# Kernel optimization log

Hardware: AMD Instinct MI355X
Metric: run time of the kernel (lower is better)

## Reference

```python
import jax, jax.numpy as jnp
import numpy as np

DIM = 256; SEQ = 2048; WIN = 64; HEADS = 4; RANK = 32; LAYERS = 3; VOCAB = 32000
EPS = 1e-6

def _unit(v):
    # unit_normalize_values: project onto unit sphere along feature dim
    return v / jnp.maximum(jnp.linalg.norm(v, axis=-1, keepdims=True), EPS)

def _signed_softmax(s):
    # signed_softmax_state: sign(s) * softmax(|s|) over nodes
    return jnp.sign(s) * jax.nn.softmax(jnp.abs(s), axis=-1)

def setup_inputs() -> dict:
    key = jax.random.key(0)
    ks = jax.random.split(key, 10)
    d = DIM
    return {
        "input_ids": jax.random.randint(ks[0], (2, SEQ), 0, VOCAB, dtype=jnp.int32),
        "emb": 0.02 * jax.random.normal(ks[1], (VOCAB, d), jnp.float32),
        "pos_emb": 0.02 * jax.random.normal(ks[2], (SEQ, d), jnp.float32),
        "anchor_val": 0.02 * jax.random.normal(ks[3], (d,), jnp.float32),
        "anchor_state": jnp.zeros((), jnp.float32),
        "Ws": 0.02 * jax.random.normal(ks[4], (d,), jnp.float32),
        "bs": jnp.zeros((), jnp.float32),
        "U": 0.02 * jax.random.normal(ks[5], (LAYERS, d, HEADS, RANK), jnp.float32),
        "V": 0.02 * jax.random.normal(ks[6], (LAYERS, d, HEADS, RANK), jnp.float32),
        "W1": 0.02 * jax.random.normal(ks[7], (LAYERS, d, 2 * d), jnp.float32),
        "b1": jnp.zeros((LAYERS, 2 * d), jnp.float32),
        "W2": 0.02 * jax.random.normal(ks[8], (LAYERS, 2 * d, d), jnp.float32),
        "b2": jnp.zeros((LAYERS, d), jnp.float32),
    }

def _forward(emb, pos_emb, anchor_val, anchor_state, Ws, bs, U, V, W1, b1, W2, b2, input_ids):
    B, S = input_ids.shape
    tok = emb[input_ids] + pos_emb[None, :S]          # [B,S,D]
    state_src = tok                                    # state projected from pre-unit-norm values
    tok = _unit(tok)
    tstate = state_src @ Ws + bs                       # [B,S] scalar state per node
    val = jnp.concatenate([jnp.broadcast_to(_unit(anchor_val), (B, 1, DIM)), tok], axis=1)
    state = jnp.concatenate([jnp.broadcast_to(anchor_state, (B, 1)), tstate], axis=1)
    N = S + 1
    offs = jnp.arange(-WIN, WIN + 1)
    idx = jnp.arange(N)[:, None] + offs[None, :]       # [N,K]
    valid = (idx >= 0) & (idx < N)
    idxc = jnp.clip(idx, 0, N - 1)
    inv_sqrt_r = np.float32(1.0 / np.sqrt(RANK))
    for l in range(LAYERS):
        q = jnp.einsum('bnd,dhr->bnhr', val, U[l])
        k = jnp.einsum('bnd,dhr->bnhr', val, V[l])
        knb = k[:, idxc]                               # [B,N,K,H,R] window gather
        s = jnp.einsum('bnhr,bnkhr->bnkh', q, knb) * inv_sqrt_r
        s = s.max(axis=-1)                             # max head-aggregate [B,N,K]
        a = jnp.where(valid, jnp.abs(s), -jnp.inf)
        wgt = jnp.where(valid, jnp.sign(s) * jax.nn.softmax(a, axis=-1), 0.0)  # signed-abs-softmax edges
        dval = jnp.einsum('bnk,bnkd->bnd', wgt, val[:, idxc])
        dstate = jnp.sum(wgt * state[:, idxc], axis=-1)
        # apply_delta: residual + norm(identity) + unit-norm + touched-mask where
        updated = val + dval
        nv = _unit(updated)
        touched = jnp.max(jnp.abs(jax.lax.stop_gradient(dval)), axis=-1, keepdims=True) > 0
        val = jnp.where(touched, nv, updated)
        state = _signed_softmax(state + dstate)
        # residual feed-forward then re-unit-norm
        h = jax.nn.gelu(jnp.einsum('bnd,dh->bnh', val, W1[l]) + b1[l], approximate=False)
        val = _unit(val + jnp.einsum('bnh,hd->bnd', h, W2[l]) + b2[l])
    return state, val

def reference(input_ids, emb, pos_emb, anchor_val, anchor_state, Ws, bs, U, V, W1, b1, W2, b2):
    return _forward(emb, pos_emb, anchor_val, anchor_state, Ws, bs, U, V, W1, b1, W2, b2, input_ids)
```

## Files before the change

kernel.cpp:

```cpp
#include <hip/hip_runtime.h>
#include <hip/hip_bf16.h>
#include <math.h>

#define BB 2
#define SS 2048
#define NN 2049
#define MM (BB*NN)
#define DD 256
#define HR 128
#define NHEAD 4
#define DFF 512
#define EPSF 1e-6f
#define TB8 257
#define EMB_BLKS 1025

typedef __attribute__((ext_vector_type(8))) short bf16x8;
typedef __attribute__((ext_vector_type(4))) float f32x4;

__device__ __forceinline__ float wave_sum(float v) {
    v += __shfl_down(v, 32, 64); v += __shfl_down(v, 16, 64);
    v += __shfl_down(v, 8, 64);  v += __shfl_down(v, 4, 64);
    v += __shfl_down(v, 2, 64);  v += __shfl_down(v, 1, 64);
    return v;
}
__device__ __forceinline__ float wave_max(float v) {
    v = fmaxf(v, __shfl_down(v, 32, 64)); v = fmaxf(v, __shfl_down(v, 16, 64));
    v = fmaxf(v, __shfl_down(v, 8, 64));  v = fmaxf(v, __shfl_down(v, 4, 64));
    v = fmaxf(v, __shfl_down(v, 2, 64));  v = fmaxf(v, __shfl_down(v, 1, 64));
    return v;
}
__device__ __forceinline__ float sgnf(float x) {
    return (x > 0.f) ? 1.f : ((x < 0.f) ? -1.f : 0.f);
}
__device__ __forceinline__ ushort f2b(float x) {
    __hip_bfloat16 h = __float2bfloat16(x);
    return *(ushort*)&h;
}
__device__ __forceinline__ float b2f(ushort u) {
    unsigned int v = ((unsigned int)u) << 16;
    return *(float*)&v;
}
__device__ __forceinline__ void split3(float x, ushort& h, ushort& m, ushort& l) {
    h = f2b(x);
    float r1 = x - b2f(h);
    m = f2b(r1);
    l = f2b(r1 - b2f(m));
}
__device__ __forceinline__ void pack_map(int e, int N, int& k, int& n) {
    int j = e & 7;
    int l = (e >> 3) & 63;
    int c = e >> 9;
    int ntiles = N >> 4;
    int kt = c / ntiles, nt = c - kt * ntiles;
    k = kt * 32 + ((l >> 4) << 3) + j;
    n = nt * 16 + (l & 15);
}


__device__ __forceinline__ void pack_job(int idx,
    const float* __restrict__ W1, const float* __restrict__ W2,
    const float* __restrict__ U,  const float* __restrict__ V,
    ushort* __restrict__ W1ph, ushort* __restrict__ W1pl,
    ushort* __restrict__ W2ph, ushort* __restrict__ W2pl,
    ushort* __restrict__ U0, ushort* __restrict__ U1, ushort* __restrict__ U2,
    ushort* __restrict__ V0, ushort* __restrict__ V1, ushort* __restrict__ V2)
{
    int l = idx / 327680;
    int r = idx - l * 327680;
    if (l >= 3) return;
    int k, n;
    if (r < 131072) {
        int e = r;
        pack_map(e, 512, k, n);
        float s = W1[(size_t)l * 131072 + (size_t)k * 512 + n];
        ushort h = f2b(s);
        W1ph[(size_t)l * 131072 + e] = h;
        W1pl[(size_t)l * 131072 + e] = f2b(s - b2f(h));
    } else if (r < 262144) {
        int e = r - 131072;
        pack_map(e, 256, k, n);
        float s = W2[(size_t)l * 131072 + (size_t)k * 256 + n];
        ushort h = f2b(s);
        W2ph[(size_t)l * 131072 + e] = h;
        W2pl[(size_t)l * 131072 + e] = f2b(s - b2f(h));
    } else if (r < 294912) {
        int e = r - 262144;
        pack_map(e, 128, k, n);
        ushort h, m, lo;
        split3(U[(size_t)l * 32768 + (size_t)k * 128 + n], h, m, lo);
        U0[(size_t)l * 32768 + e] = h;
        U1[(size_t)l * 32768 + e] = m;
        U2[(size_t)l * 32768 + e] = lo;
    } else {
        int e = r - 294912;
        pack_map(e, 128, k, n);
        ushort h, m, lo;
        split3(V[(size_t)l * 32768 + (size_t)k * 128 + n], h, m, lo);
        V0[(size_t)l * 32768 + e] = h;
        V1[(size_t)l * 32768 + e] = m;
        V2[(size_t)l * 32768 + e] = lo;
    }
}

__device__ __forceinline__ void state_job(int b, int t, float* red,
    const float* __restrict__ state_in, const float* __restrict__ dstate,
    float* __restrict__ state_out)
{
    float lmax = -INFINITY;
    for (int n = t; n < NN; n += 256) {
        float x = state_in[b * NN + n] + dstate[b * NN + n];
        lmax = fmaxf(lmax, fabsf(x));
    }
    lmax = wave_max(lmax);
    if ((t & 63) == 0) red[t >> 6] = lmax;
    __syncthreads();
    float m = fmaxf(fmaxf(red[0], red[1]), fmaxf(red[2], red[3]));
    float lsum = 0.f;
    for (int n = t; n < NN; n += 256)
        lsum += expf(fabsf(state_in[b * NN + n] + dstate[b * NN + n]) - m);
    lsum = wave_sum(lsum);
    __syncthreads();
    if ((t & 63) == 0) red[4 + (t >> 6)] = lsum;
    __syncthreads();
    float inv = 1.f / (red[4] + red[5] + red[6] + red[7]);
    for (int n = t; n < NN; n += 256) {
        float x = state_in[b * NN + n] + dstate[b * NN + n];
        state_out[b * NN + n] = sgnf(x) * expf(fabsf(x) - m) * inv;
    }
}


__global__ void pre_kernel(const int* __restrict__ ids, const float* __restrict__ emb,
                           const float* __restrict__ pos, const float* __restrict__ anchor_val,
                           const float* __restrict__ anchor_state, const float* __restrict__ Ws,
                           const float* __restrict__ bs, float* __restrict__ val,
                           float* __restrict__ state,
                           const float* __restrict__ W1, const float* __restrict__ W2,
                           const float* __restrict__ U,  const float* __restrict__ V,
                           ushort* W1ph, ushort* W1pl, ushort* W2ph, ushort* W2pl,
                           ushort* U0, ushort* U1, ushort* U2,
                           ushort* V0, ushort* V1, ushort* V2) {
    int bid = blockIdx.x;
    int t = threadIdx.x;
    if (bid < EMB_BLKS) {
        int w = t >> 6, l = t & 63;
        int row = bid * 4 + w;
        if (row >= MM) return;
        int b = row / NN, n = row % NN;
        f32x4 e;
        if (n == 0) {
            e = *(const f32x4*)(anchor_val + l * 4);
        } else {
            int id = ids[b * SS + (n - 1)];
            f32x4 em = *(const f32x4*)(emb + (size_t)id * DD + l * 4);
            f32x4 po = *(const f32x4*)(pos + (size_t)(n - 1) * DD + l * 4);
            e = em + po;
        }
        f32x4 wv = *(const f32x4*)(Ws + l * 4);
        float ss = e[0]*e[0] + e[1]*e[1] + e[2]*e[2] + e[3]*e[3];
        float ts = e[0]*wv[0] + e[1]*wv[1] + e[2]*wv[2] + e[3]*wv[3];
        #pragma unroll
        for (int off = 1; off < 64; off <<= 1) {
            ss += __shfl_xor(ss, off, 64);
            ts += __shfl_xor(ts, off, 64);
        }
        float rn = 1.f / fmaxf(sqrtf(ss), EPSF);
        f32x4 o;
        o[0] = e[0] * rn; o[1] = e[1] * rn; o[2] = e[2] * rn; o[3] = e[3] * rn;
        *(f32x4*)(val + (size_t)row * DD + l * 4) = o;
        if (l == 0) state[row] = (n == 0) ? anchor_state[0] : (ts + bs[0]);
        return;
    }
    int base = (bid - EMB_BLKS) * 1024 + t;
    #pragma unroll
    for (int k = 0; k < 4; k++)
        pack_job(base + k * 256, W1, W2, U, V,
                 W1ph, W1pl, W2ph, W2pl, U0, U1, U2, V0, V1, V2);
}


__global__ __launch_bounds__(256, 3)
void proj_kernel(const float* __restrict__ Xin,
                 const ushort* __restrict__ U0, const ushort* __restrict__ U1,
                 const ushort* __restrict__ U2,
                 const ushort* __restrict__ V0, const ushort* __restrict__ V1,
                 const ushort* __restrict__ V2,
                 ushort* __restrict__ q0, ushort* __restrict__ q1,
                 ushort* __restrict__ q2,
                 ushort* __restrict__ k0, ushort* __restrict__ k1,
                 ushort* __restrict__ k2) {
    __shared__ __align__(16) char smem[24576];
    int t = threadIdx.x;
    int w = t >> 6, l = t & 63;
    int lm = l & 15, quad = l >> 4;
    int m0 = blockIdx.x * 16;
    bool isQ = (blockIdx.y == 0);
    const ushort* P0 = isQ ? U0 : V0;
    const ushort* P1 = isQ ? U1 : V1;
    const ushort* P2 = isQ ? U2 : V2;

    #pragma unroll
    for (int rr = 0; rr < 4; rr++) {
        int row = w * 4 + rr;
        int tok = m0 + row; if (tok > MM - 1) tok = MM - 1;
        f32x4 x = *(const f32x4*)(Xin + (size_t)tok * DD + l * 4);
        ushort4 h4, m4, l4;
        ushort hh, mm, ll;
        split3(x[0], hh, mm, ll); h4.x = hh; m4.x = mm; l4.x = ll;
        split3(x[1], hh, mm, ll); h4.y = hh; m4.y = mm; l4.y = ll;
        split3(x[2], hh, mm, ll); h4.z = hh; m4.z = mm; l4.z = ll;
        split3(x[3], hh, mm, ll); h4.w = hh; m4.w = mm; l4.w = ll;
        unsigned byte = ((unsigned)(row * 512 + l * 8)) ^ ((unsigned)((row & 7) << 4));
        *(ushort4*)(smem + 0 * 8192 + byte) = h4;
        *(ushort4*)(smem + 1 * 8192 + byte) = m4;
        *(ushort4*)(smem + 2 * 8192 + byte) = l4;
    }
    __syncthreads();

    f32x4 acc[2];
    acc[0] = (f32x4)(0.f); acc[1] = (f32x4)(0.f);
    #pragma unroll
    for (int kt = 0; kt < 8; kt++) {
        unsigned abyte = ((unsigned)(lm * 512 + kt * 64 + quad * 16)) ^
                         ((unsigned)((lm & 7) << 4));
        bf16x8 a0 = *(const bf16x8*)(smem + 0 * 8192 + abyte);
        bf16x8 a1 = *(const bf16x8*)(smem + 1 * 8192 + abyte);
        bf16x8 a2 = *(const bf16x8*)(smem + 2 * 8192 + abyte);
        #pragma unroll
        for (int jj = 0; jj < 2; jj++) {
            int ntl = w * 2 + jj;
            size_t off = ((size_t)(kt * 8 + ntl) * 64 + l) * 8;
            bf16x8 b0 = *(const bf16x8*)(P0 + off);
            bf16x8 b1 = *(const bf16x8*)(P1 + off);
            bf16x8 b2 = *(const bf16x8*)(P2 + off);
            acc[jj] = __builtin_amdgcn_mfma_f32_16x16x32_bf16(a0, b0, acc[jj], 0, 0, 0);
            acc[jj] = __builtin_amdgcn_mfma_f32_16x16x32_bf16(a0, b1, acc[jj], 0, 0, 0);
            acc[jj] = __builtin_amdgcn_mfma_f32_16x16x32_bf16(a1, b0, acc[jj], 0, 0, 0);
            acc[jj] = __builtin_amdgcn_mfma_f32_16x16x32_bf16(a1, b1, acc[jj], 0, 0, 0);
            acc[jj] = __builtin_amdgcn_mfma_f32_16x16x32_bf16(a0, b2, acc[jj], 0, 0, 0);
            acc[jj] = __builtin_amdgcn_mfma_f32_16x16x32_bf16(a2, b0, acc[jj], 0, 0, 0);
        }
    }
    ushort* o0 = isQ ? q0 : k0;
    ushort* o1 = isQ ? q1 : k1;
    ushort* o2 = isQ ? q2 : k2;
    #pragma unroll
    for (int jj = 0; jj < 2; jj++) {
        int n = (w * 2 + jj) * 16 + lm;
        #pragma unroll
        for (int r = 0; r < 4; r++) {
            int tok = m0 + quad * 4 + r;
            if (tok < MM) {
                ushort h, m, lo;
                split3(acc[jj][r], h, m, lo);
                size_t oi = (size_t)tok * HR + n;
                o0[oi] = h; o1[oi] = m; o2[oi] = lo;
            }
        }
    }
}


__global__ __launch_bounds__(256, 3)
void attn_kernel(const float* __restrict__ val_in,
                 const float* __restrict__ state_in,
                 const ushort* __restrict__ q0, const ushort* __restrict__ q1,
                 const ushort* __restrict__ q2,
                 const ushort* __restrict__ k0, const ushort* __restrict__ k1,
                 const ushort* __restrict__ k2,
                 float* __restrict__ val_out,
                 ushort* __restrict__ vbH, ushort* __restrict__ vbM,
                 float* __restrict__ dstate_out) {
    __shared__ float sc4[NHEAD][8][148];
    __shared__ float wgt2[144][12];
    __shared__ float redS[8][4];
    __shared__ float redM[8][4];

    int b = blockIdx.x / TB8;
    int n0 = (blockIdx.x % TB8) * 8;
    int t = threadIdx.x;
    int w = t >> 6, l = t & 63;
    int lm = l & 15, quad = l >> 4;

    {
        int qrow = n0 + (lm & 7);
        if (qrow > NN - 1) qrow = NN - 1;
        size_t qa = ((size_t)(b * NN + qrow)) * HR + w * 32 + quad * 8;
        bf16x8 a0 = *(const bf16x8*)(q0 + qa);
        bf16x8 a1 = *(const bf16x8*)(q1 + qa);
        bf16x8 a2 = *(const bf16x8*)(q2 + qa);
        #pragma unroll
        for (int jt = 0; jt < 9; jt++) {
            int j = n0 - 64 + jt * 16 + lm;
            j = (j < 0) ? 0 : ((j > NN - 1) ? NN - 1 : j);
            size_t ka = ((size_t)(b * NN + j)) * HR + w * 32 + quad * 8;
            bf16x8 kf0 = *(const bf16x8*)(k0 + ka);
            bf16x8 kf1 = *(const bf16x8*)(k1 + ka);
            bf16x8 kf2 = *(const bf16x8*)(k2 + ka);
            f32x4 acc = (f32x4)(0.f);
            acc = __builtin_amdgcn_mfma_f32_16x16x32_bf16(a0, kf0, acc, 0, 0, 0);
            acc = __builtin_amdgcn_mfma_f32_16x16x32_bf16(a0, kf1, acc, 0, 0, 0);
            acc = __builtin_amdgcn_mfma_f32_16x16x32_bf16(a1, kf0, acc, 0, 0, 0);
            acc = __builtin_amdgcn_mfma_f32_16x16x32_bf16(a1, kf1, acc, 0, 0, 0);
            acc = __builtin_amdgcn_mfma_f32_16x16x32_bf16(a0, kf2, acc, 0, 0, 0);
            acc = __builtin_amdgcn_mfma_f32_16x16x32_bf16(a2, kf0, acc, 0, 0, 0);
            if (quad < 2) {
                #pragma unroll
                for (int r = 0; r < 4; r++)
                    sc4[w][quad * 4 + r][jt * 16 + lm] = acc[r];
            }
        }
    }
    __syncthreads();

    {
        int m = t >> 5, p = t & 31;
        int n = n0 + m;
        bool tokv = (n < NN);
        float sv[5]; bool vv[5];
        float mx = -INFINITY;
        #pragma unroll
        for (int i = 0; i < 5; i++) {
            int tap = p + 32 * i;
            bool inb = (tap < 144);
            int tapc = inb ? tap : 0;
            int j = n0 - 64 + tapc;
            float s0 = sc4[0][m][tapc], s1 = sc4[1][m][tapc];
            float s2 = sc4[2][m][tapc], s3 = sc4[3][m][tapc];
            float s = fmaxf(fmaxf(s0, s1), fmaxf(s2, s3)) * 0.17677669529663687f;
            bool v = inb && tokv && (tap >= m) && (tap <= m + 128) && (j >= 0) && (j < NN);
            sv[i] = s; vv[i] = v;
            if (v) mx = fmaxf(mx, fabsf(s));
        }
        for (int off = 16; off > 0; off >>= 1) mx = fmaxf(mx, __shfl_xor(mx, off, 64));
        float ee[5];
        float sum = 0.f;
        #pragma unroll
        for (int i = 0; i < 5; i++) {
            ee[i] = vv[i] ? expf(fabsf(sv[i]) - mx) : 0.f;
            sum += ee[i];
        }
        for (int off = 16; off > 0; off >>= 1) sum += __shfl_xor(sum, off, 64);
        float inv = (sum > 0.f) ? 1.f / sum : 0.f;
        float ds = 0.f;
        #pragma unroll
        for (int i = 0; i < 5; i++) {
            int tap = p + 32 * i;
            if (tap < 144) {
                float wg = vv[i] ? sgnf(sv[i]) * ee[i] * inv : 0.f;
                wgt2[tap][m] = wg;
                if (vv[i]) ds += wg * state_in[b * NN + (n0 - 64 + tap)];
            }
        }
        for (int off = 16; off > 0; off >>= 1) ds += __shfl_xor(ds, off, 64);
        if (p == 0 && tokv) dstate_out[b * NN + n] = ds;
    }
    __syncthreads();

    {
        int d = (t >> 2) * 4;
        int tg = t & 3;
        int tok0 = tg * 2, tok1 = tg * 2 + 1;
        int jlo = (n0 >= 64) ? 0 : (64 - n0);
        int jhi = NN - 1 - n0 + 64; if (jhi > 135) jhi = 135;
        const float* vbase = val_in + ((size_t)(b * NN + n0 - 64)) * DD + d;
        f32x4 acc0 = (f32x4)(0.f), acc1 = (f32x4)(0.f);
        int jj = jlo;
        for (; jj + 3 <= jhi; jj += 4) {
            f32x4 v0 = *(const f32x4*)(vbase + (size_t)(jj + 0) * DD);
            f32x4 v1 = *(const f32x4*)(vbase + (size_t)(jj + 1) * DD);
            f32x4 v2 = *(const f32x4*)(vbase + (size_t)(jj + 2) * DD);
            f32x4 v3 = *(const f32x4*)(vbase + (size_t)(jj + 3) * DD);
            float wa0 = wgt2[jj + 0][tok0], wa1 = wgt2[jj + 0][tok1];
            float wb0 = wgt2[jj + 1][tok0], wb1 = wgt2[jj + 1][tok1];
            float wc0 = wgt2[jj + 2][tok0], wc1 = wgt2[jj + 2][tok1];
            float wd0 = wgt2[jj + 3][tok0], wd1 = wgt2[jj + 3][tok1];
            #pragma unroll
            for (int c = 0; c < 4; c++) {
                acc0[c] += v0[c] * wa0 + v1[c] * wb0 + v2[c] * wc0 + v3[c] * wd0;
                acc1[c] += v0[c] * wa1 + v1[c] * wb1 + v2[c] * wc1 + v3[c] * wd1;
            }
        }
        for (; jj <= jhi; jj++) {
            f32x4 v = *(const f32x4*)(vbase + (size_t)jj * DD);
            float w0 = wgt2[jj][tok0], w1 = wgt2[jj][tok1];
            #pragma unroll
            for (int c = 0; c < 4; c++) {
                acc0[c] += v[c] * w0;
                acc1[c] += v[c] * w1;
            }
        }
        f32x4 u[2]; f32x4 ac[2]; ac[0] = acc0; ac[1] = acc1;
        #pragma unroll
        for (int ti = 0; ti < 2; ti++) {
            int tok = tg * 2 + ti;
            int n = n0 + tok;
            f32x4 vold = (f32x4)(0.f);
            if (n < NN) vold = *(const f32x4*)(val_in + ((size_t)(b * NN + n)) * DD + d);
            u[ti] = vold + ac[ti];
            float s = u[ti][0]*u[ti][0] + u[ti][1]*u[ti][1] + u[ti][2]*u[ti][2] + u[ti][3]*u[ti][3];
            float mb = fmaxf(fmaxf(fabsf(ac[ti][0]), fabsf(ac[ti][1])),
                             fmaxf(fabsf(ac[ti][2]), fabsf(ac[ti][3])));
            for (int off = 4; off <= 32; off <<= 1) {
                s += __shfl_xor(s, off, 64);
                mb = fmaxf(mb, __shfl_xor(mb, off, 64));
            }
            if ((l >> 2) == 0) { redS[tok][w] = s; redM[tok][w] = mb; }
        }
        __syncthreads();
        #pragma unroll
        for (int ti = 0; ti < 2; ti++) {
            int tok = tg * 2 + ti;
            int n = n0 + tok;
            if (n < NN) {
                float ss = redS[tok][0] + redS[tok][1] + redS[tok][2] + redS[tok][3];
                float mab = fmaxf(fmaxf(redM[tok][0], redM[tok][1]),
                                  fmaxf(redM[tok][2], redM[tok][3]));
                float rn = 1.f / fmaxf(sqrtf(ss), EPSF);
                f32x4 o = u[ti];
                if (mab > 0.f) { o[0] *= rn; o[1] *= rn; o[2] *= rn; o[3] *= rn; }
                size_t oi = ((size_t)(b * NN + n)) * DD + d;
                *(f32x4*)(val_out + oi) = o;
                ushort4 hv, mv;
                {
                    ushort h0 = f2b(o[0]); hv.x = h0; mv.x = f2b(o[0] - b2f(h0));
                    ushort h1 = f2b(o[1]); hv.y = h1; mv.y = f2b(o[1] - b2f(h1));
                    ushort h2 = f2b(o[2]); hv.z = h2; mv.z = f2b(o[2] - b2f(h2));
                    ushort h3 = f2b(o[3]); hv.w = h3; mv.w = f2b(o[3] - b2f(h3));
                }
                *(ushort4*)(vbH + oi) = hv;
                *(ushort4*)(vbM + oi) = mv;
            }
        }
    }
}


__global__ __launch_bounds__(1024, 1)
void fusedF_kernel(const ushort* __restrict__ vb0, const ushort* __restrict__ vb1,
                   const float*  __restrict__ valB,
                   const ushort* __restrict__ W1h, const ushort* __restrict__ W1l,
                   const float*  __restrict__ b1,
                   const ushort* __restrict__ W2h, const ushort* __restrict__ W2l,
                   const float*  __restrict__ b2,
                   const ushort* __restrict__ U0, const ushort* __restrict__ U1,
                   const ushort* __restrict__ U2,
                   const ushort* __restrict__ V0, const ushort* __restrict__ V1,
                   const ushort* __restrict__ V2,
                   ushort* __restrict__ q0, ushort* __restrict__ q1,
                   ushort* __restrict__ q2,
                   ushort* __restrict__ k0, ushort* __restrict__ k1,
                   ushort* __restrict__ k2,
                   float* __restrict__ valA,
                   const float* __restrict__ s_in, const float* __restrict__ dstate,
                   float* __restrict__ s_out,
                   float* __restrict__ out2, int last)
{
    __shared__ __align__(16) char smem[98304];
    int t = threadIdx.x;
    int bid = blockIdx.x;

    if (bid >= 129) {
        if (bid - 129 < BB) {
            if (t < 256) {
                state_job(bid - 129, t, (float*)smem, s_in, dstate, s_out);
            } else {
                __syncthreads(); __syncthreads(); __syncthreads();
            }
        }
        return;
    }

    int g  = t >> 9;
    int tl = t & 511;
    int w = tl >> 6, l = tl & 63;
    int lm = l & 15, quad = l >> 4;
    int m0 = bid * 32 + g * 16;
    int row0 = m0 + lm; if (row0 > MM - 1) row0 = MM - 1;
    char* Hh_s = smem + g * 16384;
    char* Hl_s = smem + 32768 + g * 16384;
    char* Y_s  = smem + 65536 + g * 16384;
    char* P_s  = smem + g * 24576;

    {
        const ushort* xh = vb0 + (size_t)row0 * DD + quad * 8;
        const ushort* xm = vb1 + (size_t)row0 * DD + quad * 8;
        f32x4 acc[4];
        #pragma unroll
        for (int jj = 0; jj < 4; jj++) acc[jj] = (f32x4)(0.f);
        #pragma unroll
        for (int kt = 0; kt < 8; kt++) {
            bf16x8 ah = *(const bf16x8*)(xh + kt * 32);
            bf16x8 am = *(const bf16x8*)(xm + kt * 32);
            #pragma unroll
            for (int jj = 0; jj < 4; jj++) {
                int nt = w * 4 + jj;
                size_t off = ((size_t)(kt * 32 + nt) * 64 + l) * 8;
                bf16x8 bh = *(const bf16x8*)(W1h + off);
                bf16x8 bl = *(const bf16x8*)(W1l + off);
                acc[jj] = __builtin_amdgcn_mfma_f32_16x16x32_bf16(ah, bh, acc[jj], 0, 0, 0);
                acc[jj] = __builtin_amdgcn_mfma_f32_16x16x32_bf16(am, bh, acc[jj], 0, 0, 0);
                acc[jj] = __builtin_amdgcn_mfma_f32_16x16x32_bf16(ah, bl, acc[jj], 0, 0, 0);
            }
        }
        #pragma unroll
        for (int jj = 0; jj < 4; jj++) {
            int gn = (w * 4 + jj) * 16 + lm;
            float bb = b1[gn];
            #pragma unroll
            for (int r = 0; r < 4; r++) {
                int rho = quad * 4 + r;
                float x = acc[jj][r] + bb;
                float gl = 0.5f * x * (1.f + erff(x * 0.70710678118654752f));
                ushort gh = f2b(gl);
                unsigned byte = ((unsigned)(rho * 1024 + gn * 2)) ^
                                ((unsigned)((rho & 7) << 4));
                *(ushort*)(Hh_s + byte) = gh;
                *(ushort*)(Hl_s + byte) = f2b(gl - b2f(gh));
            }
        }
    }
    __syncthreads();

    {
        f32x4 acc[2];
        acc[0] = (f32x4)(0.f); acc[1] = (f32x4)(0.f);
        #pragma unroll
        for (int kt = 0; kt < 16; kt++) {
            unsigned ab = ((unsigned)(lm * 1024 + kt * 64 + quad * 16)) ^
                          ((unsigned)((lm & 7) << 4));
            bf16x8 ah = *(const bf16x8*)(Hh_s + ab);
            bf16x8 al = *(const bf16x8*)(Hl_s + ab);
            #pragma unroll
            for (int jj = 0; jj < 2; jj++) {
                int nt = w * 2 + jj;
                size_t off = ((size_t)(kt * 16 + nt) * 64 + l) * 8;
                bf16x8 bh = *(const bf16x8*)(W2h + off);
                bf16x8 bl = *(const bf16x8*)(W2l + off);
                acc[jj] = __builtin_amdgcn_mfma_f32_16x16x32_bf16(ah, bh, acc[jj], 0, 0, 0);
                acc[jj] = __builtin_amdgcn_mfma_f32_16x16x32_bf16(al, bh, acc[jj], 0, 0, 0);
                acc[jj] = __builtin_amdgcn_mfma_f32_16x16x32_bf16(ah, bl, acc[jj], 0, 0, 0);
            }
        }
        #pragma unroll
        for (int jj = 0; jj < 2; jj++) {
            int gn = (w * 2 + jj) * 16 + lm;
            float bb = b2[gn];
            #pragma unroll
            for (int r = 0; r < 4; r++) {
                int rho = quad * 4 + r;
                int tok = m0 + rho;
                int tokc = (tok > MM - 1) ? (MM - 1) : tok;
                float y = valB[(size_t)tokc * DD + gn] + acc[jj][r] + bb;
                unsigned byte = ((unsigned)(rho * 1024 + gn * 4)) ^
                                ((unsigned)((rho & 7) << 4));
                *(float*)(Y_s + byte) = y;
            }
        }
    }
    __syncthreads();

    if (last) {
        #pragma unroll
        for (int rr = 0; rr < 2; rr++) {
            int row = w * 2 + rr;
            int tok = m0 + row;
            unsigned byte = ((unsigned)(row * 1024 + l * 16)) ^
                            ((unsigned)((row & 7) << 4));
            f32x4 y = *(const f32x4*)(Y_s + byte);
            float s = y[0]*y[0] + y[1]*y[1] + y[2]*y[2] + y[3]*y[3];
            #pragma unroll
            for (int off = 1; off < 64; off <<= 1) s += __shfl_xor(s, off, 64);
            float rn = 1.f / fmaxf(sqrtf(s), EPSF);
            if (tok < MM) {
                f32x4 o;
                o[0] = y[0] * rn; o[1] = y[1] * rn; o[2] = y[2] * rn; o[3] = y[3] * rn;
                *(f32x4*)(out2 + (size_t)tok * DD + l * 4) = o;
            }
        }
        return;
    }

    #pragma unroll
    for (int rr = 0; rr < 2; rr++) {
        int row = w * 2 + rr;
        int tok = m0 + row;
        unsigned ybyte = ((unsigned)(row * 1024 + l * 16)) ^
                         ((unsigned)((row & 7) << 4));
        f32x4 x = *(const f32x4*)(Y_s + ybyte);
        float s = x[0]*x[0] + x[1]*x[1] + x[2]*x[2] + x[3]*x[3];
        #pragma unroll
        for (int off = 1; off < 64; off <<= 1) s += __shfl_xor(s, off, 64);
        float rn = 1.f / fmaxf(sqrtf(s), EPSF);
        x[0] *= rn; x[1] *= rn; x[2] *= rn; x[3] *= rn;
        if (tok < MM) *(f32x4*)(valA + (size_t)tok * DD + l * 4) = x;
        ushort4 h4, m4, l4;
        ushort hh, mm, ll;
        split3(x[0], hh, mm, ll); h4.x = hh; m4.x = mm; l4.x = ll;
        split3(x[1], hh, mm, ll); h4.y = hh; m4.y = mm; l4.y = ll;
        split3(x[2], hh, mm, ll); h4.z = hh; m4.z = mm; l4.z = ll;
        split3(x[3], hh, mm, ll); h4.w = hh; m4.w = mm; l4.w = ll;
        unsigned pbyte = ((unsigned)(row * 512 + l * 8)) ^ ((unsigned)((row & 7) << 4));
        *(ushort4*)(P_s + 0 * 8192 + pbyte) = h4;
        *(ushort4*)(P_s + 1 * 8192 + pbyte) = m4;
        *(ushort4*)(P_s + 2 * 8192 + pbyte) = l4;
    }
    __syncthreads();

    {
        f32x4 aq = (f32x4)(0.f), ak = (f32x4)(0.f);
        #pragma unroll
        for (int kt = 0; kt < 8; kt++) {
            unsigned abyte = ((unsigned)(lm * 512 + kt * 64 + quad * 16)) ^
                             ((unsigned)((lm & 7) << 4));
            bf16x8 a0 = *(const bf16x8*)(P_s + 0 * 8192 + abyte);
            bf16x8 a1 = *(const bf16x8*)(P_s + 1 * 8192 + abyte);
            bf16x8 a2 = *(const bf16x8*)(P_s + 2 * 8192 + abyte);
            size_t off = ((size_t)(kt * 8 + w) * 64 + l) * 8;
            bf16x8 u0 = *(const bf16x8*)(U0 + off);
            bf16x8 u1 = *(const bf16x8*)(U1 + off);
            bf16x8 u2 = *(const bf16x8*)(U2 + off);
            bf16x8 v0 = *(const bf16x8*)(V0 + off);
            bf16x8 v1 = *(const bf16x8*)(V1 + off);
            bf16x8 v2 = *(const bf16x8*)(V2 + off);
            aq = __builtin_amdgcn_mfma_f32_16x16x32_bf16(a0, u0, aq, 0, 0, 0);
            ak = __builtin_amdgcn_mfma_f32_16x16x32_bf16(a0, v0, ak, 0, 0, 0);
            aq = __builtin_amdgcn_mfma_f32_16x16x32_bf16(a0, u1, aq, 0, 0, 0);
            ak = __builtin_amdgcn_mfma_f32_16x16x32_bf16(a0, v1, ak, 0, 0, 0);
            aq = __builtin_amdgcn_mfma_f32_16x16x32_bf16(a1, u0, aq, 0, 0, 0);
            ak = __builtin_amdgcn_mfma_f32_16x16x32_bf16(a1, v0, ak, 0, 0, 0);
            aq = __builtin_amdgcn_mfma_f32_16x16x32_bf16(a1, u1, aq, 0, 0, 0);
            ak = __builtin_amdgcn_mfma_f32_16x16x32_bf16(a1, v1, ak, 0, 0, 0);
            aq = __builtin_amdgcn_mfma_f32_16x16x32_bf16(a0, u2, aq, 0, 0, 0);
            ak = __builtin_amdgcn_mfma_f32_16x16x32_bf16(a0, v2, ak, 0, 0, 0);
            aq = __builtin_amdgcn_mfma_f32_16x16x32_bf16(a2, u0, aq, 0, 0, 0);
            ak = __builtin_amdgcn_mfma_f32_16x16x32_bf16(a2, v0, ak, 0, 0, 0);
        }
        int n = w * 16 + lm;
        #pragma unroll
        for (int r = 0; r < 4; r++) {
            int tok = m0 + quad * 4 + r;
            if (tok < MM) {
                ushort h, m, lo;
                size_t oi = (size_t)tok * HR + n;
                split3(aq[r], h, m, lo);
                q0[oi] = h; q1[oi] = m; q2[oi] = lo;
                split3(ak[r], h, m, lo);
                k0[oi] = h; k1[oi] = m; k2[oi] = lo;
            }
        }
    }
}


extern "C" void kernel_launch(void* const* d_in, const int* in_sizes, int n_in,
                              void* d_out, int out_size, void* d_ws, size_t ws_size,
                              hipStream_t stream) {
    const int*   ids          = (const int*)d_in[0];
    const float* emb          = (const float*)d_in[1];
    const float* pos          = (const float*)d_in[2];
    const float* anchor_val   = (const float*)d_in[3];
    const float* anchor_state = (const float*)d_in[4];
    const float* Ws           = (const float*)d_in[5];
    const float* bs           = (const float*)d_in[6];
    const float* U            = (const float*)d_in[7];
    const float* V            = (const float*)d_in[8];
    const float* W1           = (const float*)d_in[9];
    const float* b1           = (const float*)d_in[10];
    const float* W2           = (const float*)d_in[11];
    const float* b2           = (const float*)d_in[12];
    float* out = (float*)d_out;

    ushort* p = (ushort*)d_ws;
    ushort* vB0 = p; p += (size_t)MM * DD;
    ushort* vB1 = p; p += (size_t)MM * DD;
    ushort* q0b = p; p += (size_t)MM * HR;
    ushort* q1b = p; p += (size_t)MM * HR;
    ushort* q2b = p; p += (size_t)MM * HR;
    ushort* k0b = p; p += (size_t)MM * HR;
    ushort* k1b = p; p += (size_t)MM * HR;
    ushort* k2b = p; p += (size_t)MM * HR;
    ushort* W1ph = p; p += 3 * 131072;
    ushort* W1pl = p; p += 3 * 131072;
    ushort* W2ph = p; p += 3 * 131072;
    ushort* W2pl = p; p += 3 * 131072;
    ushort* U0p = p; p += 3 * 32768;
    ushort* U1p = p; p += 3 * 32768;
    ushort* U2p = p; p += 3 * 32768;
    ushort* V0p = p; p += 3 * 32768;
    ushort* V1p = p; p += 3 * 32768;
    ushort* V2p = p; p += 3 * 32768;
    float* f = (float*)p;
    float* valA = f; f += (size_t)MM * DD;
    float* valB = f; f += (size_t)MM * DD;
    float* st0  = f; f += MM;
    float* st1  = f; f += MM;
    float* dst  = f; f += MM;

    pre_kernel<<<EMB_BLKS + 960, 256, 0, stream>>>(ids, emb, pos, anchor_val, anchor_state,
                                                   Ws, bs, valA, st0,
                                                   W1, W2, U, V,
                                                   W1ph, W1pl, W2ph, W2pl,
                                                   U0p, U1p, U2p, V0p, V1p, V2p);
    proj_kernel<<<dim3(257, 2), 256, 0, stream>>>(
        valA, U0p, U1p, U2p, V0p, V1p, V2p,
        q0b, q1b, q2b, k0b, k1b, k2b);

    float* s_in = st0;
    float* s_out = st1;
    for (int l = 0; l < 3; l++) {
        attn_kernel<<<BB * TB8, 256, 0, stream>>>(valA, s_in,
                                                  q0b, q1b, q2b, k0b, k1b, k2b,
                                                  valB, vB0, vB1, dst);
        int ln = (l < 2) ? (l + 1) : 0;
        fusedF_kernel<<<131, 1024, 0, stream>>>(
            vB0, vB1, valB,
            W1ph + (size_t)l * 131072, W1pl + (size_t)l * 131072, b1 + (size_t)l * DFF,
            W2ph + (size_t)l * 131072, W2pl + (size_t)l * 131072, b2 + (size_t)l * DD,
            U0p + (size_t)ln * 32768, U1p + (size_t)ln * 32768, U2p + (size_t)ln * 32768,
            V0p + (size_t)ln * 32768, V1p + (size_t)ln * 32768, V2p + (size_t)ln * 32768,
            q0b, q1b, q2b, k0b, k1b, k2b,
            valA,
            s_in, dst, (l == 2) ? out : s_out,
            out + MM, (l == 2) ? 1 : 0);
        float* tmp = s_in; s_in = s_out; s_out = tmp;
    }
}
```

Before: 298.6 us.

## Fuse attention and feed-forward per layer into one kernel via shared memory

Merges the windowed attention kernel and the fused feed-forward/projection kernel into one 1024-thread layer kernel. Each block runs four attention tiles of 8 tokens and stages the updated values and their bf16 hi/mid splits in shared memory for the FFN and next-layer Q/K projection, so the valB/vB0/vB1 global round trip is gone. Q/K and value buffers are now double-buffered, because other blocks still read the previous layer's neighbours. The state softmax moves into a separate small kernel. In exchange, only 129 blocks of 1024 threads run, with about 129KB of shared memory each, which cuts the parallelism available to the attention phase.

```diff
diff --git a/kernel.cpp b/kernel.cpp
--- a/kernel.cpp
+++ b/kernel.cpp
@@ -12,6 +12,8 @@
 #define DFF 512
 #define EPSF 1e-6f
 #define TB8 257
+#define NTILE 514
+#define MBLK 129
 #define EMB_BLKS 1025
 
 typedef __attribute__((ext_vector_type(8))) short bf16x8;
@@ -261,31 +263,53 @@
 }
 
 
-__global__ __launch_bounds__(256, 3)
-void attn_kernel(const float* __restrict__ val_in,
-                 const float* __restrict__ state_in,
-                 const ushort* __restrict__ q0, const ushort* __restrict__ q1,
-                 const ushort* __restrict__ q2,
-                 const ushort* __restrict__ k0, const ushort* __restrict__ k1,
-                 const ushort* __restrict__ k2,
-                 float* __restrict__ val_out,
-                 ushort* __restrict__ vbH, ushort* __restrict__ vbM,
-                 float* __restrict__ dstate_out) {
-    __shared__ float sc4[NHEAD][8][148];
-    __shared__ float wgt2[144][12];
-    __shared__ float redS[8][4];
-    __shared__ float redM[8][4];
-
-    int b = blockIdx.x / TB8;
-    int n0 = (blockIdx.x % TB8) * 8;
+__global__ void state_kernel(const float* __restrict__ s_in,
+                             const float* __restrict__ dstate,
+                             float* __restrict__ s_out) {
+    __shared__ float red[8];
+    state_job(blockIdx.x, threadIdx.x, red, s_in, dstate, s_out);
+}
+
+
+__global__ __launch_bounds__(1024, 1)
+void layer_kernel(const float* __restrict__ valA, const float* __restrict__ s_in,
+                  const ushort* __restrict__ q0, const ushort* __restrict__ q1,
+                  const ushort* __restrict__ q2,
+                  const ushort* __restrict__ k0, const ushort* __restrict__ k1,
+                  const ushort* __restrict__ k2,
+                  const ushort* __restrict__ W1h, const ushort* __restrict__ W1l,
+                  const float*  __restrict__ b1,
+                  const ushort* __restrict__ W2h, const ushort* __restrict__ W2l,
+                  const float*  __restrict__ b2,
+                  const ushort* __restrict__ U0, const ushort* __restrict__ U1,
+                  const ushort* __restrict__ U2,
+                  const ushort* __restrict__ V0, const ushort* __restrict__ V1,
+                  const ushort* __restrict__ V2,
+                  ushort* __restrict__ oq0, ushort* __restrict__ oq1,
+                  ushort* __restrict__ oq2,
+                  ushort* __restrict__ ok0, ushort* __restrict__ ok1,
+                  ushort* __restrict__ ok2,
+                  float* __restrict__ valA_out, float* __restrict__ dstate_out,
+                  float* __restrict__ out2, int last)
+{
+    __shared__ __align__(16) char smem[132096];
     int t = threadIdx.x;
-    int w = t >> 6, l = t & 63;
-    int lm = l & 15, quad = l >> 4;
+    int bid = blockIdx.x;
+
+    int tb4 = t >> 8;
+    int tl  = t & 255;
+    int tile = 4 * bid + tb4;
+    int treal = (tile < NTILE) ? tile : (NTILE - 1);
+    int batt = (treal >= 257) ? 1 : 0;
+    int n0 = (treal - batt * 257) * 8;
 
     {
+        float* sc4 = (float*)(smem + tb4 * 18944);
+        int w = tl >> 6, l = tl & 63;
+        int lm = l & 15, quad = l >> 4;
         int qrow = n0 + (lm & 7);
         if (qrow > NN - 1) qrow = NN - 1;
-        size_t qa = ((size_t)(b * NN + qrow)) * HR + w * 32 + quad * 8;
+        size_t qa = ((size_t)(batt * NN + qrow)) * HR + w * 32 + quad * 8;
         bf16x8 a0 = *(const bf16x8*)(q0 + qa);
         bf16x8 a1 = *(const bf16x8*)(q1 + qa);
         bf16x8 a2 = *(const bf16x8*)(q2 + qa);
@@ -293,7 +317,7 @@
         for (int jt = 0; jt < 9; jt++) {
             int j = n0 - 64 + jt * 16 + lm;
             j = (j < 0) ? 0 : ((j > NN - 1) ? NN - 1 : j);
-            size_t ka = ((size_t)(b * NN + j)) * HR + w * 32 + quad * 8;
+            size_t ka = ((size_t)(batt * NN + j)) * HR + w * 32 + quad * 8;
             bf16x8 kf0 = *(const bf16x8*)(k0 + ka);
             bf16x8 kf1 = *(const bf16x8*)(k1 + ka);
             bf16x8 kf2 = *(const bf16x8*)(k2 + ka);
@@ -307,14 +331,16 @@
             if (quad < 2) {
                 #pragma unroll
                 for (int r = 0; r < 4; r++)
-                    sc4[w][quad * 4 + r][jt * 16 + lm] = acc[r];
+                    sc4[((size_t)w * 8 + quad * 4 + r) * 148 + jt * 16 + lm] = acc[r];
             }
         }
     }
     __syncthreads();
 
     {
-        int m = t >> 5, p = t & 31;
+        float* sc4  = (float*)(smem + tb4 * 18944);
+        float* wgt2 = (float*)(smem + 75776 + tb4 * 6912);
+        int m = tl >> 5, p = tl & 31;
         int n = n0 + m;
         bool tokv = (n < NN);
         float sv[5]; bool vv[5];
@@ -325,8 +351,8 @@
             bool inb = (tap < 144);
             int tapc = inb ? tap : 0;
             int j = n0 - 64 + tapc;
-            float s0 = sc4[0][m][tapc], s1 = sc4[1][m][tapc];
-            float s2 = sc4[2][m][tapc], s3 = sc4[3][m][tapc];
+            float s0 = sc4[(0 * 8 + m) * 148 + tapc], s1 = sc4[(1 * 8 + m) * 148 + tapc];
+            float s2 = sc4[(2 * 8 + m) * 148 + tapc], s3 = sc4[(3 * 8 + m) * 148 + tapc];
             float s = fmaxf(fmaxf(s0, s1), fmaxf(s2, s3)) * 0.17677669529663687f;
             bool v = inb && tokv && (tap >= m) && (tap <= m + 128) && (j >= 0) && (j < NN);
             sv[i] = s; vv[i] = v;
@@ -348,22 +374,26 @@
             int tap = p + 32 * i;
             if (tap < 144) {
                 float wg = vv[i] ? sgnf(sv[i]) * ee[i] * inv : 0.f;
-                wgt2[tap][m] = wg;
-                if (vv[i]) ds += wg * state_in[b * NN + (n0 - 64 + tap)];
+                wgt2[tap * 12 + m] = wg;
+                if (vv[i]) ds += wg * s_in[batt * NN + (n0 - 64 + tap)];
             }
         }
         for (int off = 16; off > 0; off >>= 1) ds += __shfl_xor(ds, off, 64);
-        if (p == 0 && tokv) dstate_out[b * NN + n] = ds;
+        if (p == 0 && tokv && tile < NTILE) dstate_out[batt * NN + n] = ds;
     }
     __syncthreads();
 
     {
-        int d = (t >> 2) * 4;
-        int tg = t & 3;
+        float* wgt2 = (float*)(smem + 75776 + tb4 * 6912);
+        float* redS = (float*)(smem + 131072 + tb4 * 256);
+        float* redM = redS + 32;
+        int w = tl >> 6, l = tl & 63;
+        int d = (tl >> 2) * 4;
+        int tg = tl & 3;
         int tok0 = tg * 2, tok1 = tg * 2 + 1;
         int jlo = (n0 >= 64) ? 0 : (64 - n0);
         int jhi = NN - 1 - n0 + 64; if (jhi > 135) jhi = 135;
-        const float* vbase = val_in + ((size_t)(b * NN + n0 - 64)) * DD + d;
+        const float* vbase = valA + ((size_t)(batt * NN + n0 - 64)) * DD + d;
         f32x4 acc0 = (f32x4)(0.f), acc1 = (f32x4)(0.f);
         int jj = jlo;
         for (; jj + 3 <= jhi; jj += 4) {
@@ -371,10 +401,10 @@
             f32x4 v1 = *(const f32x4*)(vbase + (size_t)(jj + 1) * DD);
             f32x4 v2 = *(const f32x4*)(vbase + (size_t)(jj + 2) * DD);
             f32x4 v3 = *(const f32x4*)(vbase + (size_t)(jj + 3) * DD);
-            float wa0 = wgt2[jj + 0][tok0], wa1 = wgt2[jj + 0][tok1];
-            float wb0 = wgt2[jj + 1][tok0], wb1 = wgt2[jj + 1][tok1];
-            float wc0 = wgt2[jj + 2][tok0], wc1 = wgt2[jj + 2][tok1];
-            float wd0 = wgt2[jj + 3][tok0], wd1 = wgt2[jj + 3][tok1];
+            float wa0 = wgt2[(jj + 0) * 12 + tok0], wa1 = wgt2[(jj + 0) * 12 + tok1];
+            float wb0 = wgt2[(jj + 1) * 12 + tok0], wb1 = wgt2[(jj + 1) * 12 + tok1];
+            float wc0 = wgt2[(jj + 2) * 12 + tok0], wc1 = wgt2[(jj + 2) * 12 + tok1];
+            float wd0 = wgt2[(jj + 3) * 12 + tok0], wd1 = wgt2[(jj + 3) * 12 + tok1];
             #pragma unroll
             for (int c = 0; c < 4; c++) {
                 acc0[c] += v0[c] * wa0 + v1[c] * wb0 + v2[c] * wc0 + v3[c] * wd0;
@@ -383,7 +413,7 @@
         }
         for (; jj <= jhi; jj++) {
             f32x4 v = *(const f32x4*)(vbase + (size_t)jj * DD);
-            float w0 = wgt2[jj][tok0], w1 = wgt2[jj][tok1];
+            float w0 = wgt2[jj * 12 + tok0], w1 = wgt2[jj * 12 + tok1];
             #pragma unroll
             for (int c = 0; c < 4; c++) {
                 acc0[c] += v[c] * w0;
@@ -396,7 +426,7 @@
             int tok = tg * 2 + ti;
             int n = n0 + tok;
             f32x4 vold = (f32x4)(0.f);
-            if (n < NN) vold = *(const f32x4*)(val_in + ((size_t)(b * NN + n)) * DD + d);
+            if (n < NN) vold = *(const f32x4*)(valA + ((size_t)(batt * NN + n)) * DD + d);
             u[ti] = vold + ac[ti];
             float s = u[ti][0]*u[ti][0] + u[ti][1]*u[ti][1] + u[ti][2]*u[ti][2] + u[ti][3]*u[ti][3];
             float mb = fmaxf(fmaxf(fabsf(ac[ti][0]), fabsf(ac[ti][1])),
@@ -405,93 +435,60 @@
                 s += __shfl_xor(s, off, 64);
                 mb = fmaxf(mb, __shfl_xor(mb, off, 64));
             }
-            if ((l >> 2) == 0) { redS[tok][w] = s; redM[tok][w] = mb; }
+            if ((l >> 2) == 0) { redS[tok * 4 + w] = s; redM[tok * 4 + w] = mb; }
         }
         __syncthreads();
         #pragma unroll
         for (int ti = 0; ti < 2; ti++) {
             int tok = tg * 2 + ti;
+            int slot = tb4 * 8 + tok;
             int n = n0 + tok;
+            f32x4 o = (f32x4)(0.f);
             if (n < NN) {
-                float ss = redS[tok][0] + redS[tok][1] + redS[tok][2] + redS[tok][3];
-                float mab = fmaxf(fmaxf(redM[tok][0], redM[tok][1]),
-                                  fmaxf(redM[tok][2], redM[tok][3]));
+                float ss = redS[tok * 4 + 0] + redS[tok * 4 + 1] + redS[tok * 4 + 2] + redS[tok * 4 + 3];
+                float mab = fmaxf(fmaxf(redM[tok * 4 + 0], redM[tok * 4 + 1]),
+                                  fmaxf(redM[tok * 4 + 2], redM[tok * 4 + 3]));
                 float rn = 1.f / fmaxf(sqrtf(ss), EPSF);
-                f32x4 o = u[ti];
+                o = u[ti];
                 if (mab > 0.f) { o[0] *= rn; o[1] *= rn; o[2] *= rn; o[3] *= rn; }
-                size_t oi = ((size_t)(b * NN + n)) * DD + d;
-                *(f32x4*)(val_out + oi) = o;
-                ushort4 hv, mv;
-                {
-                    ushort h0 = f2b(o[0]); hv.x = h0; mv.x = f2b(o[0] - b2f(h0));
-                    ushort h1 = f2b(o[1]); hv.y = h1; mv.y = f2b(o[1] - b2f(h1));
-                    ushort h2 = f2b(o[2]); hv.z = h2; mv.z = f2b(o[2] - b2f(h2));
-                    ushort h3 = f2b(o[3]); hv.w = h3; mv.w = f2b(o[3] - b2f(h3));
-                }
-                *(ushort4*)(vbH + oi) = hv;
-                *(ushort4*)(vbM + oi) = mv;
-            }
-        }
-    }
-}
-
-
-__global__ __launch_bounds__(1024, 1)
-void fusedF_kernel(const ushort* __restrict__ vb0, const ushort* __restrict__ vb1,
-                   const float*  __restrict__ valB,
-                   const ushort* __restrict__ W1h, const ushort* __restrict__ W1l,
-                   const float*  __restrict__ b1,
-                   const ushort* __restrict__ W2h, const ushort* __restrict__ W2l,
-                   const float*  __restrict__ b2,
-                   const ushort* __restrict__ U0, const ushort* __restrict__ U1,
-                   const ushort* __restrict__ U2,
-                   const ushort* __restrict__ V0, const ushort* __restrict__ V1,
-                   const ushort* __restrict__ V2,
-                   ushort* __restrict__ q0, ushort* __restrict__ q1,
-                   ushort* __restrict__ q2,
-                   ushort* __restrict__ k0, ushort* __restrict__ k1,
-                   ushort* __restrict__ k2,
-                   float* __restrict__ valA,
-                   const float* __restrict__ s_in, const float* __restrict__ dstate,
-                   float* __restrict__ s_out,
-                   float* __restrict__ out2, int last)
-{
-    __shared__ __align__(16) char smem[98304];
-    int t = threadIdx.x;
-    int bid = blockIdx.x;
-
-    if (bid >= 129) {
-        if (bid - 129 < BB) {
-            if (t < 256) {
-                state_job(bid - 129, t, (float*)smem, s_in, dstate, s_out);
-            } else {
-                __syncthreads(); __syncthreads(); __syncthreads();
-            }
-        }
-        return;
-    }
-
-    int g  = t >> 9;
-    int tl = t & 511;
-    int w = tl >> 6, l = tl & 63;
+            }
+            unsigned vbb = ((unsigned)(slot * 1024 + d * 4)) ^ ((unsigned)((slot & 7) << 4));
+            *(f32x4*)(smem + vbb) = o;
+            ushort4 hv, mv;
+            {
+                ushort h0 = f2b(o[0]); hv.x = h0; mv.x = f2b(o[0] - b2f(h0));
+                ushort h1 = f2b(o[1]); hv.y = h1; mv.y = f2b(o[1] - b2f(h1));
+                ushort h2 = f2b(o[2]); hv.z = h2; mv.z = f2b(o[2] - b2f(h2));
+                ushort h3 = f2b(o[3]); hv.w = h3; mv.w = f2b(o[3] - b2f(h3));
+            }
+            unsigned pb = ((unsigned)(slot * 512 + d * 2)) ^ ((unsigned)((slot & 7) << 4));
+            *(ushort4*)(smem + 32768 + pb) = hv;
+            *(ushort4*)(smem + 49152 + pb) = mv;
+        }
+    }
+    __syncthreads();
+
+    int g   = t >> 9;
+    int tg2 = t & 511;
+    int w = tg2 >> 6, l = tg2 & 63;
     int lm = l & 15, quad = l >> 4;
-    int m0 = bid * 32 + g * 16;
-    int row0 = m0 + lm; if (row0 > MM - 1) row0 = MM - 1;
-    char* Hh_s = smem + g * 16384;
-    char* Hl_s = smem + 32768 + g * 16384;
-    char* Y_s  = smem + 65536 + g * 16384;
-    char* P_s  = smem + g * 24576;
+    char* Hh_s = smem + 65536 + g * 16384;
+    char* Hl_s = smem + 98304 + g * 16384;
+    char* Y_s  = smem + 32768 + g * 16384;
+    char* P_s  = smem + 65536 + g * 24576;
 
     {
-        const ushort* xh = vb0 + (size_t)row0 * DD + quad * 8;
-        const ushort* xm = vb1 + (size_t)row0 * DD + quad * 8;
+        int slot = g * 16 + lm;
+        unsigned sxor = (unsigned)((slot & 7) << 4);
+        unsigned vb0b = (unsigned)(slot * 512);
         f32x4 acc[4];
         #pragma unroll
         for (int jj = 0; jj < 4; jj++) acc[jj] = (f32x4)(0.f);
         #pragma unroll
         for (int kt = 0; kt < 8; kt++) {
-            bf16x8 ah = *(const bf16x8*)(xh + kt * 32);
-            bf16x8 am = *(const bf16x8*)(xm + kt * 32);
+            unsigned ab = (vb0b + kt * 64 + quad * 16) ^ sxor;
+            bf16x8 ah = *(const bf16x8*)(smem + 32768 + ab);
+            bf16x8 am = *(const bf16x8*)(smem + 49152 + ab);
             #pragma unroll
             for (int jj = 0; jj < 4; jj++) {
                 int nt = w * 4 + jj;
@@ -549,9 +546,10 @@
             #pragma unroll
             for (int r = 0; r < 4; r++) {
                 int rho = quad * 4 + r;
-                int tok = m0 + rho;
-                int tokc = (tok > MM - 1) ? (MM - 1) : tok;
-                float y = valB[(size_t)tokc * DD + gn] + acc[jj][r] + bb;
+                int slot = g * 16 + rho;
+                unsigned rb = ((unsigned)(slot * 1024 + gn * 4)) ^
+                              ((unsigned)((slot & 7) << 4));
+                float y = *(const float*)(smem + rb) + acc[jj][r] + bb;
                 unsigned byte = ((unsigned)(rho * 1024 + gn * 4)) ^
                                 ((unsigned)((rho & 7) << 4));
                 *(float*)(Y_s + byte) = y;
@@ -564,7 +562,13 @@
         #pragma unroll
         for (int rr = 0; rr < 2; rr++) {
             int row = w * 2 + rr;
-            int tok = m0 + row;
+            int slot = g * 16 + row;
+            int ts = 4 * bid + (slot >> 3);
+            int tsc = (ts < NTILE) ? ts : (NTILE - 1);
+            int bts = (tsc >= 257) ? 1 : 0;
+            int n0s = (tsc - bts * 257) * 8;
+            int nn = n0s + (slot & 7);
+            bool vld = (ts < NTILE) && (nn < NN);
             unsigned byte = ((unsigned)(row * 1024 + l * 16)) ^
                             ((unsigned)((row & 7) << 4));
             f32x4 y = *(const f32x4*)(Y_s + byte);
@@ -572,10 +576,11 @@
             #pragma unroll
             for (int off = 1; off < 64; off <<= 1) s += __shfl_xor(s, off, 64);
             float rn = 1.f / fmaxf(sqrtf(s), EPSF);
-            if (tok < MM) {
+            if (vld) {
+                int grow = bts * NN + nn;
                 f32x4 o;
                 o[0] = y[0] * rn; o[1] = y[1] * rn; o[2] = y[2] * rn; o[3] = y[3] * rn;
-                *(f32x4*)(out2 + (size_t)tok * DD + l * 4) = o;
+                *(f32x4*)(out2 + (size_t)grow * DD + l * 4) = o;
             }
         }
         return;
@@ -584,7 +589,13 @@
     #pragma unroll
     for (int rr = 0; rr < 2; rr++) {
         int row = w * 2 + rr;
-        int tok = m0 + row;
+        int slot = g * 16 + row;
+        int ts = 4 * bid + (slot >> 3);
+        int tsc = (ts < NTILE) ? ts : (NTILE - 1);
+        int bts = (tsc >= 257) ? 1 : 0;
+        int n0s = (tsc - bts * 257) * 8;
+        int nn = n0s + (slot & 7);
+        bool vld = (ts < NTILE) && (nn < NN);
         unsigned ybyte = ((unsigned)(row * 1024 + l * 16)) ^
                          ((unsigned)((row & 7) << 4));
         f32x4 x = *(const f32x4*)(Y_s + ybyte);
@@ -593,7 +604,10 @@
         for (int off = 1; off < 64; off <<= 1) s += __shfl_xor(s, off, 64);
         float rn = 1.f / fmaxf(sqrtf(s), EPSF);
         x[0] *= rn; x[1] *= rn; x[2] *= rn; x[3] *= rn;
-        if (tok < MM) *(f32x4*)(valA + (size_t)tok * DD + l * 4) = x;
+        if (vld) {
+            int grow = bts * NN + nn;
+            *(f32x4*)(valA_out + (size_t)grow * DD + l * 4) = x;
+        }
         ushort4 h4, m4, l4;
         ushort hh, mm, ll;
         split3(x[0], hh, mm, ll); h4.x = hh; m4.x = mm; l4.x = ll;
@@ -639,14 +653,21 @@
         int n = w * 16 + lm;
         #pragma unroll
         for (int r = 0; r < 4; r++) {
-            int tok = m0 + quad * 4 + r;
-            if (tok < MM) {
+            int slot = g * 16 + quad * 4 + r;
+            int ts = 4 * bid + (slot >> 3);
+            int tsc = (ts < NTILE) ? ts : (NTILE - 1);
+            int bts = (tsc >= 257) ? 1 : 0;
+            int n0s = (tsc - bts * 257) * 8;
+            int nn = n0s + (slot & 7);
+            bool vld = (ts < NTILE) && (nn < NN);
+            if (vld) {
+                int grow = bts * NN + nn;
                 ushort h, m, lo;
-                size_t oi = (size_t)tok * HR + n;
+                size_t oi = (size_t)grow * HR + n;
                 split3(aq[r], h, m, lo);
-                q0[oi] = h; q1[oi] = m; q2[oi] = lo;
+                oq0[oi] = h; oq1[oi] = m; oq2[oi] = lo;
                 split3(ak[r], h, m, lo);
-                k0[oi] = h; k1[oi] = m; k2[oi] = lo;
+                ok0[oi] = h; ok1[oi] = m; ok2[oi] = lo;
             }
         }
     }
@@ -672,14 +693,8 @@
     float* out = (float*)d_out;
 
     ushort* p = (ushort*)d_ws;
-    ushort* vB0 = p; p += (size_t)MM * DD;
-    ushort* vB1 = p; p += (size_t)MM * DD;
-    ushort* q0b = p; p += (size_t)MM * HR;
-    ushort* q1b = p; p += (size_t)MM * HR;
-    ushort* q2b = p; p += (size_t)MM * HR;
-    ushort* k0b = p; p += (size_t)MM * HR;
-    ushort* k1b = p; p += (size_t)MM * HR;
-    ushort* k2b = p; p += (size_t)MM * HR;
+    ushort* qkA = p; p += (size_t)6 * MM * HR;
+    ushort* qkB = p; p += (size_t)6 * MM * HR;
     ushort* W1ph = p; p += 3 * 131072;
     ushort* W1pl = p; p += 3 * 131072;
     ushort* W2ph = p; p += 3 * 131072;
@@ -691,38 +706,47 @@
     ushort* V1p = p; p += 3 * 32768;
     ushort* V2p = p; p += 3 * 32768;
     float* f = (float*)p;
-    float* valA = f; f += (size_t)MM * DD;
-    float* valB = f; f += (size_t)MM * DD;
+    float* valA0 = f; f += (size_t)MM * DD;
+    float* valA1 = f; f += (size_t)MM * DD;
     float* st0  = f; f += MM;
     float* st1  = f; f += MM;
     float* dst  = f; f += MM;
 
+    ushort* S0[6], *S1[6];
+    for (int i = 0; i < 6; i++) {
+        S0[i] = qkA + (size_t)i * MM * HR;
+        S1[i] = qkB + (size_t)i * MM * HR;
+    }
+
     pre_kernel<<<EMB_BLKS + 960, 256, 0, stream>>>(ids, emb, pos, anchor_val, anchor_state,
-                                                   Ws, bs, valA, st0,
+                                                   Ws, bs, valA0, st0,
                                                    W1, W2, U, V,
                                                    W1ph, W1pl, W2ph, W2pl,
                                                    U0p, U1p, U2p, V0p, V1p, V2p);
     proj_kernel<<<dim3(257, 2), 256, 0, stream>>>(
-        valA, U0p, U1p, U2p, V0p, V1p, V2p,
-        q0b, q1b, q2b, k0b, k1b, k2b);
+        valA0, U0p, U1p, U2p, V0p, V1p, V2p,
+        S0[0], S0[1], S0[2], S0[3], S0[4], S0[5]);
 
     float* s_in = st0;
     float* s_out = st1;
     for (int l = 0; l < 3; l++) {
-        attn_kernel<<<BB * TB8, 256, 0, stream>>>(valA, s_in,
-                                                  q0b, q1b, q2b, k0b, k1b, k2b,
-                                                  valB, vB0, vB1, dst);
+        int par = l & 1;
+        float* vin  = par ? valA1 : valA0;
+        float* vout = par ? valA0 : valA1;
+        ushort** qin  = par ? S1 : S0;
+        ushort** qout = par ? S0 : S1;
         int ln = (l < 2) ? (l + 1) : 0;
-        fusedF_kernel<<<131, 1024, 0, stream>>>(
-            vB0, vB1, valB,
+        layer_kernel<<<MBLK, 1024, 0, stream>>>(
+            vin, s_in,
+            qin[0], qin[1], qin[2], qin[3], qin[4], qin[5],
             W1ph + (size_t)l * 131072, W1pl + (size_t)l * 131072, b1 + (size_t)l * DFF,
             W2ph + (size_t)l * 131072, W2pl + (size_t)l * 131072, b2 + (size_t)l * DD,
             U0p + (size_t)ln * 32768, U1p + (size_t)ln * 32768, U2p + (size_t)ln * 32768,
             V0p + (size_t)ln * 32768, V1p + (size_t)ln * 32768, V2p + (size_t)ln * 32768,
-            q0b, q1b, q2b, k0b, k1b, k2b,
-            valA,
-            s_in, dst, (l == 2) ? out : s_out,
+            qout[0], qout[1], qout[2], qout[3], qout[4], qout[5],
+            vout, dst,
             out + MM, (l == 2) ? 1 : 0);
+        state_kernel<<<BB, 256, 0, stream>>>(s_in, dst, (l == 2) ? out : s_out);
         float* tmp = s_in; s_in = s_out; s_out = tmp;
     }
 }
```

New measurement: 313.7 us. 1.05x slower.

## Stage W1 tiles into LDS with double-buffered async global-to-LDS loads

Applied to the files above, without the earlier changes.

In the fused FFN kernel, the W1 hi/lo bf16 tiles are no longer read from global memory by each wave. They are copied into a double-buffered LDS staging area with global_load_lds 16-byte DMA, and the next k-slice is prefetched while the current one feeds the MFMAs. Both 16-row groups of the block share the staged tile, which is meant to cut redundant global/L2 traffic and hide load latency. In exchange it adds a block-wide barrier per k-step and grows the shared buffer to 128 KB, which may limit occupancy.

```diff
diff --git a/kernel.cpp b/kernel.cpp
--- a/kernel.cpp
+++ b/kernel.cpp
@@ -54,6 +54,12 @@
     int kt = c / ntiles, nt = c - kt * ntiles;
     k = kt * 32 + ((l >> 4) << 3) + j;
     n = nt * 16 + (l & 15);
+}
+__device__ __forceinline__ void dma16(const ushort* g, ushort* lds) {
+    __builtin_amdgcn_global_load_lds(
+        (const __attribute__((address_space(1))) unsigned int*)g,
+        (__attribute__((address_space(3))) unsigned int*)lds,
+        16, 0, 0);
 }
 
 
@@ -456,7 +462,7 @@
                    float* __restrict__ s_out,
                    float* __restrict__ out2, int last)
 {
-    __shared__ __align__(16) char smem[98304];
+    __shared__ __align__(16) char smem[131072];
     int t = threadIdx.x;
     int bid = blockIdx.x;
 
@@ -474,6 +480,7 @@
     int g  = t >> 9;
     int tl = t & 511;
     int w = tl >> 6, l = tl & 63;
+    int wg = t >> 6;
     int lm = l & 15, quad = l >> 4;
     int m0 = bid * 32 + g * 16;
     int row0 = m0 + lm; if (row0 > MM - 1) row0 = MM - 1;
@@ -488,21 +495,45 @@
         f32x4 acc[4];
         #pragma unroll
         for (int jj = 0; jj < 4; jj++) acc[jj] = (f32x4)(0.f);
+
+        #pragma unroll
+        for (int i = 0; i < 4; i++) {
+            int pp = wg * 4 + i;
+            int plane = pp >> 5, nt = pp & 31;
+            const ushort* src = (plane ? W1l : W1h) + (size_t)(0 * 32 + nt) * 512 + l * 8;
+            dma16(src, (ushort*)(smem + plane * 32768 + nt * 1024) + l * 8);
+        }
+        __syncthreads();
+
         #pragma unroll
         for (int kt = 0; kt < 8; kt++) {
+            int cur = kt & 1;
+            if (kt < 7) {
+                #pragma unroll
+                for (int i = 0; i < 4; i++) {
+                    int pp = wg * 4 + i;
+                    int plane = pp >> 5, nt = pp & 31;
+                    const ushort* src = (plane ? W1l : W1h) +
+                        (size_t)((kt + 1) * 32 + nt) * 512 + l * 8;
+                    dma16(src, (ushort*)(smem + (cur ^ 1) * 65536 +
+                                         plane * 32768 + nt * 1024) + l * 8);
+                }
+            }
             bf16x8 ah = *(const bf16x8*)(xh + kt * 32);
             bf16x8 am = *(const bf16x8*)(xm + kt * 32);
+            char* stg = smem + cur * 65536;
             #pragma unroll
             for (int jj = 0; jj < 4; jj++) {
                 int nt = w * 4 + jj;
-                size_t off = ((size_t)(kt * 32 + nt) * 64 + l) * 8;
-                bf16x8 bh = *(const bf16x8*)(W1h + off);
-                bf16x8 bl = *(const bf16x8*)(W1l + off);
+                bf16x8 bh = *(const bf16x8*)(stg + nt * 1024 + l * 16);
+                bf16x8 bl = *(const bf16x8*)(stg + 32768 + nt * 1024 + l * 16);
                 acc[jj] = __builtin_amdgcn_mfma_f32_16x16x32_bf16(ah, bh, acc[jj], 0, 0, 0);
                 acc[jj] = __builtin_amdgcn_mfma_f32_16x16x32_bf16(am, bh, acc[jj], 0, 0, 0);
                 acc[jj] = __builtin_amdgcn_mfma_f32_16x16x32_bf16(ah, bl, acc[jj], 0, 0, 0);
             }
-        }
+            __syncthreads();
+        }
+
         #pragma unroll
         for (int jj = 0; jj < 4; jj++) {
             int gn = (w * 4 + jj) * 16 + lm;
```

Result: no change. 295.8 us (-0.9%).
